# Performance work log

Measured on AMD Instinct MI355X. Metric: run time of the kernel, lower is better.

The kernel has to match this reference:

```python
import jax, jax.numpy as jnp
import numpy as np


def setup_inputs() -> dict:
    key = jax.random.key(0)
    k_u, k_dt, k_A, k_B, k_C = jax.random.split(key, 5)
    batch, seq_len, d_model = 8, 4096, 1024
    u = jax.random.normal(k_u, (batch, seq_len, d_model), dtype=jnp.float32)
    # delta is a positive discretization step size
    delta = jax.random.uniform(k_dt, (batch, seq_len, d_model), dtype=jnp.float32,
                               minval=0.001, maxval=0.1)
    # A initialized in [-1.0, -0.1] so exp(A*delta) in (0,1) (stable decay)
    A = jax.random.uniform(k_A, (d_model,), dtype=jnp.float32, minval=-1.0, maxval=-0.1)
    B = jax.random.normal(k_B, (batch, seq_len, d_model), dtype=jnp.float32)
    C = jax.random.normal(k_C, (batch, seq_len, d_model), dtype=jnp.float32)
    return {"u": u, "delta": delta, "A": A, "B": B, "C": C}


def _selective_scan(u, delta, A, B, C):
    # Per-channel SSM with scalar state (N=1):
    #   a_t = exp(A * delta_t)           (decay factor, in (0,1))
    #   h_t = a_t * h_{t-1} + delta_t * B_t * u_t
    #   y_t = C_t * h_t
    a = jnp.exp(delta * A)          # [b, s, d]
    b = delta * B * u               # [b, s, d]

    def combine(left, right):
        a1, b1 = left
        a2, b2 = right
        return a1 * a2, a2 * b1 + b2

    _, h = jax.lax.associative_scan(combine, (a, b), axis=1)  # [b, s, d]
    return C * h


def reference(u, delta, A, B, C):
    return _selective_scan(u, delta, A, B, C)
```

## Files before the change

kernel.cpp:

```cpp
#include <hip/hip_runtime.h>


#define BB 8
#define SS 4096
#define DD 1024
#define TT 16
#define NCHUNK (SS / TT)
#define NBLK   (BB * NCHUNK)

typedef __attribute__((ext_vector_type(4))) float f32x4;

__device__ __forceinline__ float4 ld4(const float* __restrict__ p) {
    return *(const float4*)p;
}

__device__ __forceinline__ void scan_step(float4& h, float4& p,
                                          const float4 dt, const float4 bv,
                                          const float4 uv, const float4 Av) {
    float a;
    a = __expf(dt.x * Av.x); h.x = fmaf(a, h.x, dt.x * bv.x * uv.x); p.x *= a;
    a = __expf(dt.y * Av.y); h.y = fmaf(a, h.y, dt.y * bv.y * uv.y); p.y *= a;
    a = __expf(dt.z * Av.z); h.z = fmaf(a, h.z, dt.z * bv.z * uv.z); p.z *= a;
    a = __expf(dt.w * Av.w); h.w = fmaf(a, h.w, dt.w * bv.w * uv.w); p.w *= a;
}

__global__ __launch_bounds__(256) void k1_local(
    const float* __restrict__ u, const float* __restrict__ delta,
    const float* __restrict__ A, const float* __restrict__ Bm,
    float* __restrict__ aggA, float* __restrict__ aggB)
{
    const int c = blockIdx.x % NCHUNK;
    const int b = blockIdx.x / NCHUNK;
    const int d4 = threadIdx.x << 2;

    const float4 Av = ld4(A + d4);
    const size_t base = ((size_t)(b * SS + c * TT)) * DD + d4;

    float4 h = {0.f, 0.f, 0.f, 0.f};
    float4 p = {1.f, 1.f, 1.f, 1.f};

    float4 dt[3], bv[3], uv[3];
    dt[0] = ld4(delta + base);      bv[0] = ld4(Bm + base);      uv[0] = ld4(u + base);
    dt[1] = ld4(delta + base + DD); bv[1] = ld4(Bm + base + DD); uv[1] = ld4(u + base + DD);
#pragma unroll
    for (int t = 0; t < TT; ++t) {
        if (t + 2 < TT) {
            const int s2 = (t + 2) % 3;
            const size_t i2 = base + (size_t)(t + 2) * DD;
            dt[s2] = ld4(delta + i2);
            bv[s2] = ld4(Bm + i2);
            uv[s2] = ld4(u + i2);
        }
        const int s = t % 3;
        scan_step(h, p, dt[s], bv[s], uv[s], Av);
    }
    const size_t o = ((size_t)(b * NCHUNK + c)) * DD + d4;
    *(float4*)(aggA + o) = p;
    *(float4*)(aggB + o) = h;
}

__global__ __launch_bounds__(64) void k2_scan(
    const float* __restrict__ aggA, const float* __restrict__ aggB,
    float* __restrict__ pref)
{
    const int b = blockIdx.x >> 4;
    const int d = ((blockIdx.x & 15) << 6) + threadIdx.x;
    const size_t base = (size_t)b * NCHUNK * DD + (size_t)d;

    float X = 0.f;
#pragma unroll 8
    for (int c = 0; c < NCHUNK; ++c) {
        const size_t o = base + (size_t)c * DD;
        pref[o] = X;
        X = fmaf(aggA[o], X, aggB[o]);
    }
}

__global__ __launch_bounds__(256) void k3_apply(
    const float* __restrict__ u, const float* __restrict__ delta,
    const float* __restrict__ A, const float* __restrict__ Bm,
    const float* __restrict__ Cm, const float* __restrict__ pref,
    float* __restrict__ out)
{
    const int c = blockIdx.x % NCHUNK;
    const int b = blockIdx.x / NCHUNK;
    const int d4 = threadIdx.x << 2;

    const float4 Av = ld4(A + d4);
    float4 h = ld4(pref + ((size_t)(b * NCHUNK + c)) * DD + d4);
    const size_t base = ((size_t)(b * SS + c * TT)) * DD + d4;

    float4 dt[3], bv[3], uv[3], cv[2];
    float4 dump = {0.f, 0.f, 0.f, 0.f};
    dt[0] = ld4(delta + base);      bv[0] = ld4(Bm + base);      uv[0] = ld4(u + base);
    dt[1] = ld4(delta + base + DD); bv[1] = ld4(Bm + base + DD); uv[1] = ld4(u + base + DD);
    cv[0] = ld4(Cm + base);
#pragma unroll
    for (int t = 0; t < TT; ++t) {
        if (t + 2 < TT) {
            const int s2 = (t + 2) % 3;
            const size_t i2 = base + (size_t)(t + 2) * DD;
            dt[s2] = ld4(delta + i2);
            bv[s2] = ld4(Bm + i2);
            uv[s2] = ld4(u + i2);
        }
        if (t + 1 < TT) cv[(t + 1) % 2] = ld4(Cm + base + (size_t)(t + 1) * DD);
        const int s = t % 3;
        scan_step(h, dump, dt[s], bv[s], uv[s], Av);
        const float4 c4 = cv[t % 2];
        f32x4 y;
        y.x = c4.x * h.x; y.y = c4.y * h.y; y.z = c4.z * h.z; y.w = c4.w * h.w;
        __builtin_nontemporal_store(y, (f32x4*)(out + base + (size_t)t * DD));
    }
}

extern "C" void kernel_launch(void* const* d_in, const int* in_sizes, int n_in,
                              void* d_out, int out_size, void* d_ws, size_t ws_size,
                              hipStream_t stream) {
    (void)in_sizes; (void)n_in; (void)out_size; (void)ws_size;
    const float* u     = (const float*)d_in[0];
    const float* delta = (const float*)d_in[1];
    const float* A     = (const float*)d_in[2];
    const float* Bm    = (const float*)d_in[3];
    const float* Cm    = (const float*)d_in[4];
    float* out = (float*)d_out;

    float* ws = (float*)d_ws;
    const size_t n = (size_t)BB * NCHUNK * DD;
    float* aggA = ws;
    float* aggB = ws + n;
    float* pref = ws + 2 * n;

    k1_local<<<NBLK, 256, 0, stream>>>(u, delta, A, Bm, aggA, aggB);
    k2_scan<<<BB * (DD / 64), 64, 0, stream>>>(aggA, aggB, pref);
    k3_apply<<<NBLK, 256, 0, stream>>>(u, delta, A, Bm, Cm, pref, out);
}
```

Before: 244.8 us.

## Process two chunks per block, reverse k3 block order, nontemporal C loads

```diff
diff --git a/kernel.cpp b/kernel.cpp
--- a/kernel.cpp
+++ b/kernel.cpp
@@ -6,22 +6,35 @@
 #define DD 1024
 #define TT 16
 #define NCHUNK (SS / TT)
-#define NBLK   (BB * NCHUNK)
+#define NPAIR  (NCHUNK / 2)
+#define NBLK2  (BB * NPAIR)
 
 typedef __attribute__((ext_vector_type(4))) float f32x4;
 
-__device__ __forceinline__ float4 ld4(const float* __restrict__ p) {
-    return *(const float4*)p;
+__device__ __forceinline__ f32x4 ld4(const float* __restrict__ p) {
+    return *(const f32x4*)p;
+}
+__device__ __forceinline__ f32x4 ntld4(const float* __restrict__ p) {
+    return __builtin_nontemporal_load((const f32x4*)p);
 }
 
-__device__ __forceinline__ void scan_step(float4& h, float4& p,
-                                          const float4 dt, const float4 bv,
-                                          const float4 uv, const float4 Av) {
+__device__ __forceinline__ void step_p(f32x4& h, f32x4& p,
+                                       const f32x4 dt, const f32x4 bv,
+                                       const f32x4 uv, const f32x4 Av) {
     float a;
     a = __expf(dt.x * Av.x); h.x = fmaf(a, h.x, dt.x * bv.x * uv.x); p.x *= a;
     a = __expf(dt.y * Av.y); h.y = fmaf(a, h.y, dt.y * bv.y * uv.y); p.y *= a;
     a = __expf(dt.z * Av.z); h.z = fmaf(a, h.z, dt.z * bv.z * uv.z); p.z *= a;
     a = __expf(dt.w * Av.w); h.w = fmaf(a, h.w, dt.w * bv.w * uv.w); p.w *= a;
+}
+__device__ __forceinline__ void step_np(f32x4& h,
+                                        const f32x4 dt, const f32x4 bv,
+                                        const f32x4 uv, const f32x4 Av) {
+    float a;
+    a = __expf(dt.x * Av.x); h.x = fmaf(a, h.x, dt.x * bv.x * uv.x);
+    a = __expf(dt.y * Av.y); h.y = fmaf(a, h.y, dt.y * bv.y * uv.y);
+    a = __expf(dt.z * Av.z); h.z = fmaf(a, h.z, dt.z * bv.z * uv.z);
+    a = __expf(dt.w * Av.w); h.w = fmaf(a, h.w, dt.w * bv.w * uv.w);
 }
 
 __global__ __launch_bounds__(256) void k1_local(
@@ -29,34 +42,30 @@
     const float* __restrict__ A, const float* __restrict__ Bm,
     float* __restrict__ aggA, float* __restrict__ aggB)
 {
-    const int c = blockIdx.x % NCHUNK;
-    const int b = blockIdx.x / NCHUNK;
-    const int d4 = threadIdx.x << 2;
+    const int pair = blockIdx.x % NPAIR;
+    const int b    = blockIdx.x / NPAIR;
+    const int c0   = pair * 2;
+    const int d4   = threadIdx.x << 2;
 
-    const float4 Av = ld4(A + d4);
-    const size_t base = ((size_t)(b * SS + c * TT)) * DD + d4;
+    const f32x4 Av = ld4(A + d4);
+    size_t i0 = ((size_t)(b * SS + c0 * TT)) * DD + d4;
+    size_t i1 = i0 + (size_t)TT * DD;
 
-    float4 h = {0.f, 0.f, 0.f, 0.f};
-    float4 p = {1.f, 1.f, 1.f, 1.f};
-
-    float4 dt[3], bv[3], uv[3];
-    dt[0] = ld4(delta + base);      bv[0] = ld4(Bm + base);      uv[0] = ld4(u + base);
-    dt[1] = ld4(delta + base + DD); bv[1] = ld4(Bm + base + DD); uv[1] = ld4(u + base + DD);
+    f32x4 h0 = {0.f,0.f,0.f,0.f}, p0 = {1.f,1.f,1.f,1.f};
+    f32x4 h1 = {0.f,0.f,0.f,0.f}, p1 = {1.f,1.f,1.f,1.f};
 #pragma unroll
-    for (int t = 0; t < TT; ++t) {
-        if (t + 2 < TT) {
-            const int s2 = (t + 2) % 3;
-            const size_t i2 = base + (size_t)(t + 2) * DD;
-            dt[s2] = ld4(delta + i2);
-            bv[s2] = ld4(Bm + i2);
-            uv[s2] = ld4(u + i2);
-        }
-        const int s = t % 3;
-        scan_step(h, p, dt[s], bv[s], uv[s], Av);
+    for (int t = 0; t < TT; ++t, i0 += DD, i1 += DD) {
+        const f32x4 dt0 = ld4(delta + i0), dt1 = ld4(delta + i1);
+        const f32x4 bv0 = ld4(Bm + i0),    bv1 = ld4(Bm + i1);
+        const f32x4 uv0 = ld4(u + i0),     uv1 = ld4(u + i1);
+        step_p(h0, p0, dt0, bv0, uv0, Av);
+        step_p(h1, p1, dt1, bv1, uv1, Av);
     }
-    const size_t o = ((size_t)(b * NCHUNK + c)) * DD + d4;
-    *(float4*)(aggA + o) = p;
-    *(float4*)(aggB + o) = h;
+    const size_t o0 = ((size_t)(b * NCHUNK + c0)) * DD + d4;
+    *(f32x4*)(aggA + o0) = p0;
+    *(f32x4*)(aggB + o0) = h0;
+    *(f32x4*)(aggA + o0 + DD) = p1;
+    *(f32x4*)(aggB + o0 + DD) = h1;
 }
 
 __global__ __launch_bounds__(64) void k2_scan(
@@ -68,7 +77,7 @@
     const size_t base = (size_t)b * NCHUNK * DD + (size_t)d;
 
     float X = 0.f;
-#pragma unroll 8
+#pragma unroll 32
     for (int c = 0; c < NCHUNK; ++c) {
         const size_t o = base + (size_t)c * DD;
         pref[o] = X;
@@ -82,35 +91,32 @@
     const float* __restrict__ Cm, const float* __restrict__ pref,
     float* __restrict__ out)
 {
-    const int c = blockIdx.x % NCHUNK;
-    const int b = blockIdx.x / NCHUNK;
-    const int d4 = threadIdx.x << 2;
+    const int rbid = (NBLK2 - 1) - blockIdx.x;
+    const int pair = rbid % NPAIR;
+    const int b    = rbid / NPAIR;
+    const int c0   = pair * 2;
+    const int d4   = threadIdx.x << 2;
 
-    const float4 Av = ld4(A + d4);
-    float4 h = ld4(pref + ((size_t)(b * NCHUNK + c)) * DD + d4);
-    const size_t base = ((size_t)(b * SS + c * TT)) * DD + d4;
+    const f32x4 Av = ld4(A + d4);
+    const size_t o0 = ((size_t)(b * NCHUNK + c0)) * DD + d4;
+    f32x4 h0 = ld4(pref + o0);
+    f32x4 h1 = ld4(pref + o0 + DD);
 
-    float4 dt[3], bv[3], uv[3], cv[2];
-    float4 dump = {0.f, 0.f, 0.f, 0.f};
-    dt[0] = ld4(delta + base);      bv[0] = ld4(Bm + base);      uv[0] = ld4(u + base);
-    dt[1] = ld4(delta + base + DD); bv[1] = ld4(Bm + base + DD); uv[1] = ld4(u + base + DD);
-    cv[0] = ld4(Cm + base);
+    size_t i0 = ((size_t)(b * SS + c0 * TT)) * DD + d4;
+    size_t i1 = i0 + (size_t)TT * DD;
 #pragma unroll
-    for (int t = 0; t < TT; ++t) {
-        if (t + 2 < TT) {
-            const int s2 = (t + 2) % 3;
-            const size_t i2 = base + (size_t)(t + 2) * DD;
-            dt[s2] = ld4(delta + i2);
-            bv[s2] = ld4(Bm + i2);
-            uv[s2] = ld4(u + i2);
-        }
-        if (t + 1 < TT) cv[(t + 1) % 2] = ld4(Cm + base + (size_t)(t + 1) * DD);
-        const int s = t % 3;
-        scan_step(h, dump, dt[s], bv[s], uv[s], Av);
-        const float4 c4 = cv[t % 2];
-        f32x4 y;
-        y.x = c4.x * h.x; y.y = c4.y * h.y; y.z = c4.z * h.z; y.w = c4.w * h.w;
-        __builtin_nontemporal_store(y, (f32x4*)(out + base + (size_t)t * DD));
+    for (int t = 0; t < TT; ++t, i0 += DD, i1 += DD) {
+        const f32x4 dt0 = ld4(delta + i0), dt1 = ld4(delta + i1);
+        const f32x4 bv0 = ld4(Bm + i0),    bv1 = ld4(Bm + i1);
+        const f32x4 uv0 = ld4(u + i0),     uv1 = ld4(u + i1);
+        const f32x4 cv0 = ntld4(Cm + i0),  cv1 = ntld4(Cm + i1);
+        step_np(h0, dt0, bv0, uv0, Av);
+        step_np(h1, dt1, bv1, uv1, Av);
+        f32x4 y0, y1;
+        y0.x = cv0.x * h0.x; y0.y = cv0.y * h0.y; y0.z = cv0.z * h0.z; y0.w = cv0.w * h0.w;
+        y1.x = cv1.x * h1.x; y1.y = cv1.y * h1.y; y1.z = cv1.z * h1.z; y1.w = cv1.w * h1.w;
+        __builtin_nontemporal_store(y0, (f32x4*)(out + i0));
+        __builtin_nontemporal_store(y1, (f32x4*)(out + i1));
     }
 }
 
@@ -131,7 +137,7 @@
     float* aggB = ws + n;
     float* pref = ws + 2 * n;
 
-    k1_local<<<NBLK, 256, 0, stream>>>(u, delta, A, Bm, aggA, aggB);
+    k1_local<<<NBLK2, 256, 0, stream>>>(u, delta, A, Bm, aggA, aggB);
     k2_scan<<<BB * (DD / 64), 64, 0, stream>>>(aggA, aggB, pref);
-    k3_apply<<<NBLK, 256, 0, stream>>>(u, delta, A, Bm, Cm, pref, out);
+    k3_apply<<<NBLK2, 256, 0, stream>>>(u, delta, A, Bm, Cm, pref, out);
 }
```

New measurement: 275.1 us. 12.4% more time.

## Reverse k3 block order for cache reuse, simplify loads, nontemporal C loads

Applied to the files above, without the earlier changes.

```diff
diff --git a/kernel.cpp b/kernel.cpp
--- a/kernel.cpp
+++ b/kernel.cpp
@@ -10,18 +10,11 @@
 
 typedef __attribute__((ext_vector_type(4))) float f32x4;
 
-__device__ __forceinline__ float4 ld4(const float* __restrict__ p) {
-    return *(const float4*)p;
+__device__ __forceinline__ f32x4 ld4(const float* __restrict__ p) {
+    return *(const f32x4*)p;
 }
-
-__device__ __forceinline__ void scan_step(float4& h, float4& p,
-                                          const float4 dt, const float4 bv,
-                                          const float4 uv, const float4 Av) {
-    float a;
-    a = __expf(dt.x * Av.x); h.x = fmaf(a, h.x, dt.x * bv.x * uv.x); p.x *= a;
-    a = __expf(dt.y * Av.y); h.y = fmaf(a, h.y, dt.y * bv.y * uv.y); p.y *= a;
-    a = __expf(dt.z * Av.z); h.z = fmaf(a, h.z, dt.z * bv.z * uv.z); p.z *= a;
-    a = __expf(dt.w * Av.w); h.w = fmaf(a, h.w, dt.w * bv.w * uv.w); p.w *= a;
+__device__ __forceinline__ f32x4 ntld4(const float* __restrict__ p) {
+    return __builtin_nontemporal_load((const f32x4*)p);
 }
 
 __global__ __launch_bounds__(256) void k1_local(
@@ -33,30 +26,25 @@
     const int b = blockIdx.x / NCHUNK;
     const int d4 = threadIdx.x << 2;
 
-    const float4 Av = ld4(A + d4);
-    const size_t base = ((size_t)(b * SS + c * TT)) * DD + d4;
+    const f32x4 Av = ld4(A + d4);
+    size_t idx = ((size_t)(b * SS + c * TT)) * DD + d4;
 
-    float4 h = {0.f, 0.f, 0.f, 0.f};
-    float4 p = {1.f, 1.f, 1.f, 1.f};
-
-    float4 dt[3], bv[3], uv[3];
-    dt[0] = ld4(delta + base);      bv[0] = ld4(Bm + base);      uv[0] = ld4(u + base);
-    dt[1] = ld4(delta + base + DD); bv[1] = ld4(Bm + base + DD); uv[1] = ld4(u + base + DD);
+    f32x4 h = {0.f, 0.f, 0.f, 0.f};
+    f32x4 p = {1.f, 1.f, 1.f, 1.f};
 #pragma unroll
-    for (int t = 0; t < TT; ++t) {
-        if (t + 2 < TT) {
-            const int s2 = (t + 2) % 3;
-            const size_t i2 = base + (size_t)(t + 2) * DD;
-            dt[s2] = ld4(delta + i2);
-            bv[s2] = ld4(Bm + i2);
-            uv[s2] = ld4(u + i2);
-        }
-        const int s = t % 3;
-        scan_step(h, p, dt[s], bv[s], uv[s], Av);
+    for (int t = 0; t < TT; ++t, idx += DD) {
+        const f32x4 dt = ld4(delta + idx);
+        const f32x4 bv = ld4(Bm + idx);
+        const f32x4 uv = ld4(u + idx);
+        float a;
+        a = __expf(dt.x * Av.x); h.x = fmaf(a, h.x, dt.x * bv.x * uv.x); p.x *= a;
+        a = __expf(dt.y * Av.y); h.y = fmaf(a, h.y, dt.y * bv.y * uv.y); p.y *= a;
+        a = __expf(dt.z * Av.z); h.z = fmaf(a, h.z, dt.z * bv.z * uv.z); p.z *= a;
+        a = __expf(dt.w * Av.w); h.w = fmaf(a, h.w, dt.w * bv.w * uv.w); p.w *= a;
     }
     const size_t o = ((size_t)(b * NCHUNK + c)) * DD + d4;
-    *(float4*)(aggA + o) = p;
-    *(float4*)(aggB + o) = h;
+    *(f32x4*)(aggA + o) = p;
+    *(f32x4*)(aggB + o) = h;
 }
 
 __global__ __launch_bounds__(64) void k2_scan(
@@ -68,7 +56,7 @@
     const size_t base = (size_t)b * NCHUNK * DD + (size_t)d;
 
     float X = 0.f;
-#pragma unroll 8
+#pragma unroll 32
     for (int c = 0; c < NCHUNK; ++c) {
         const size_t o = base + (size_t)c * DD;
         pref[o] = X;
@@ -82,35 +70,28 @@
     const float* __restrict__ Cm, const float* __restrict__ pref,
     float* __restrict__ out)
 {
-    const int c = blockIdx.x % NCHUNK;
-    const int b = blockIdx.x / NCHUNK;
+    const int rbid = (NBLK - 1) - (int)blockIdx.x;
+    const int c = rbid % NCHUNK;
+    const int b = rbid / NCHUNK;
     const int d4 = threadIdx.x << 2;
 
-    const float4 Av = ld4(A + d4);
-    float4 h = ld4(pref + ((size_t)(b * NCHUNK + c)) * DD + d4);
-    const size_t base = ((size_t)(b * SS + c * TT)) * DD + d4;
-
-    float4 dt[3], bv[3], uv[3], cv[2];
-    float4 dump = {0.f, 0.f, 0.f, 0.f};
-    dt[0] = ld4(delta + base);      bv[0] = ld4(Bm + base);      uv[0] = ld4(u + base);
-    dt[1] = ld4(delta + base + DD); bv[1] = ld4(Bm + base + DD); uv[1] = ld4(u + base + DD);
-    cv[0] = ld4(Cm + base);
+    const f32x4 Av = ld4(A + d4);
+    f32x4 h = ld4(pref + ((size_t)(b * NCHUNK + c)) * DD + d4);
+    size_t idx = ((size_t)(b * SS + c * TT)) * DD + d4;
 #pragma unroll
-    for (int t = 0; t < TT; ++t) {
-        if (t + 2 < TT) {
-            const int s2 = (t + 2) % 3;
-            const size_t i2 = base + (size_t)(t + 2) * DD;
-            dt[s2] = ld4(delta + i2);
-            bv[s2] = ld4(Bm + i2);
-            uv[s2] = ld4(u + i2);
-        }
-        if (t + 1 < TT) cv[(t + 1) % 2] = ld4(Cm + base + (size_t)(t + 1) * DD);
-        const int s = t % 3;
-        scan_step(h, dump, dt[s], bv[s], uv[s], Av);
-        const float4 c4 = cv[t % 2];
+    for (int t = 0; t < TT; ++t, idx += DD) {
+        const f32x4 dt = ld4(delta + idx);
+        const f32x4 bv = ld4(Bm + idx);
+        const f32x4 uv = ld4(u + idx);
+        const f32x4 cv = ntld4(Cm + idx);
+        float a;
+        a = __expf(dt.x * Av.x); h.x = fmaf(a, h.x, dt.x * bv.x * uv.x);
+        a = __expf(dt.y * Av.y); h.y = fmaf(a, h.y, dt.y * bv.y * uv.y);
+        a = __expf(dt.z * Av.z); h.z = fmaf(a, h.z, dt.z * bv.z * uv.z);
+        a = __expf(dt.w * Av.w); h.w = fmaf(a, h.w, dt.w * bv.w * uv.w);
         f32x4 y;
-        y.x = c4.x * h.x; y.y = c4.y * h.y; y.z = c4.z * h.z; y.w = c4.w * h.w;
-        __builtin_nontemporal_store(y, (f32x4*)(out + base + (size_t)t * DD));
+        y.x = cv.x * h.x; y.y = cv.y * h.y; y.z = cv.z * h.z; y.w = cv.w * h.w;
+        __builtin_nontemporal_store(y, (f32x4*)(out + idx));
     }
 }
 
```

Result: slower. 285.8 us (+16.8%).
